# Optimization experiments

Hardware: AMD Instinct MI355X
Metric: run time of the kernel (lower is better)

## Reference

```python
import jax, jax.numpy as jnp
import numpy as np

FP8_MAX = 448.0      # max normal of float8_e4m3fn
BLOCK = 128          # TPUGEMMLinear.block_size default
INFO_THRESHOLD = 0.1
NUM_PATHS = 4


def act_quant(x, block=BLOCK):
    """Block-wise fp8 quantization along the last dim. Returns (q, scale) with
    q fp8_e4m3 of shape [..., n_blocks, block] and scale [..., n_blocks, 1]."""
    b = min(block, x.shape[-1])
    xb = x.reshape(*x.shape[:-1], x.shape[-1] // b, b)
    scale = jnp.max(jnp.abs(xb), axis=-1, keepdims=True) / FP8_MAX
    scale = jnp.maximum(scale, 1e-12)  # avoid div-by-zero
    xq = (xb / scale).astype(jnp.float8_e4m3fn)
    return xq, scale


def dequant(xq, scale, shape):
    return (xq.astype(jnp.float32) * scale).reshape(shape)


def quantize_roundtrip(x):
    xq, xs = act_quant(x)
    return dequant(xq, xs, x.shape)


def setup_inputs() -> dict:
    key = jax.random.key(0)
    k_x, k_ik, k_pk = jax.random.split(key, 3)
    N, D, F, P = 32768, 1024, 1024, NUM_PATHS
    Fp = F // P
    x = jax.random.normal(k_x, (N, D), dtype=jnp.float32)
    # lecun_normal init: std = 1/sqrt(fan_in)
    info_kernel = jax.random.normal(k_ik, (D, P), dtype=jnp.float32) / np.sqrt(D)
    info_bias = jnp.zeros((P,), dtype=jnp.float32)
    path_kernels = jax.random.normal(k_pk, (P, D, Fp), dtype=jnp.float32) / np.sqrt(D)
    path_biases = jnp.zeros((P, Fp), dtype=jnp.float32)
    return {"x": x, "info_kernel": info_kernel, "info_bias": info_bias,
            "path_kernels": path_kernels, "path_biases": path_biases}


def reference(x, info_kernel, info_bias, path_kernels, path_biases):
    N, D = x.shape
    P = info_kernel.shape[-1]
    # fp8 quantize/dequant round trips (simulated fp8 GEMM: dequant then matmul)
    xd = quantize_roundtrip(x)                      # [N, D]
    ikd = quantize_roundtrip(info_kernel)           # [D, P]
    pkd = quantize_roundtrip(path_kernels)          # [P, D, Fp]
    # info-gain gating
    info_net = xd @ ikd + info_bias                 # [N, P]
    info_gains = jax.nn.sigmoid(info_net)
    cumul_info = info_gains                         # prev_info defaults to zeros
    # training=True: soft path weights
    path_weights = jax.nn.sigmoid((cumul_info - INFO_THRESHOLD) * 10.0)  # [N, P]
    # per-path projections (batched GEMM) + per-path chunk weighting
    path_out = jnp.einsum('nd,pdf->npf', xd, pkd) + path_biases          # [N, P, Fp]
    out = (path_out * path_weights[:, :, None]).reshape(N, -1)           # [N, F]
    return out, cumul_info
```

## Files before the change

kernel.cpp:

```cpp
#include <hip/hip_runtime.h>
#include <hip/hip_bf16.h>
#include <stdint.h>


typedef float v2f __attribute__((ext_vector_type(2)));
typedef float f32x4 __attribute__((ext_vector_type(4)));
typedef __bf16 bf16x8 __attribute__((ext_vector_type(8)));
typedef unsigned short us4 __attribute__((ext_vector_type(4)));

__device__ __forceinline__ unsigned short f2bf(float f) {
  unsigned u = __builtin_bit_cast(unsigned, f);
  u += 0x7fffu + ((u >> 16) & 1u);
  return (unsigned short)(u >> 16);
}

__device__ __forceinline__ v2f fp8_rt2s(float a, float b, float sa, float sb) {
  int q = __builtin_amdgcn_cvt_pk_fp8_f32(a / sa, b / sb, 0, false);
  v2f r = __builtin_amdgcn_cvt_pk_f32_fp8(q, false);
  r.x *= sa;
  r.y *= sb;
  return r;
}

__device__ __forceinline__ void g2l16(const void* g, void* l) {
  __builtin_amdgcn_global_load_lds(
      (const __attribute__((address_space(1))) unsigned int*)g,
      (__attribute__((address_space(3))) unsigned int*)l,
      16, 0, 0);
}

__global__ __launch_bounds__(256) void k_quant_info(
    const float* __restrict__ x, const float* __restrict__ ik,
    const float* __restrict__ ib, unsigned short* __restrict__ xd,
    float* __restrict__ pw, float* __restrict__ cumul, int N) {
  __shared__ f32x4 s_ik[1024];
  const int tid = threadIdx.x;

  for (int d = tid; d < 1024; d += 256) {
    f32x4 v = ((const f32x4*)ik)[d];
    float m = fmaxf(fmaxf(fabsf(v.x), fabsf(v.y)), fmaxf(fabsf(v.z), fabsf(v.w)));
    float s = fmaxf(m * (1.0f / 448.0f), 1e-12f);
    v2f lo = fp8_rt2s(v.x, v.y, s, s);
    v2f hi = fp8_rt2s(v.z, v.w, s, s);
    f32x4 dq;
    dq.x = lo.x; dq.y = lo.y; dq.z = hi.x; dq.w = hi.y;
    s_ik[d] = dq;
  }
  __syncthreads();

  const int lane = tid & 63, wv = tid >> 6;
  const int gw = blockIdx.x * 4 + wv;
  const int nw = gridDim.x * 4;
  const f32x4 ibv = *(const f32x4*)ib;

  for (int row = gw; row < N; row += nw) {
    const f32x4* xr = (const f32x4*)(x + (size_t)row * 1024);
    float p0 = 0.f, p1 = 0.f, p2 = 0.f, p3 = 0.f;
#pragma unroll
    for (int j = 0; j < 4; ++j) {
      f32x4 v = xr[j * 64 + lane];
      float m = fmaxf(fmaxf(fabsf(v.x), fabsf(v.y)), fmaxf(fabsf(v.z), fabsf(v.w)));
#pragma unroll
      for (int off = 1; off <= 16; off <<= 1)
        m = fmaxf(m, __shfl_xor(m, off, 64));
      float s = fmaxf(m * (1.0f / 448.0f), 1e-12f);
      v2f lo = fp8_rt2s(v.x, v.y, s, s);
      v2f hi = fp8_rt2s(v.z, v.w, s, s);
      const int e = j * 256 + lane * 4;
      us4 h;
      h.x = f2bf(lo.x); h.y = f2bf(lo.y); h.z = f2bf(hi.x); h.w = f2bf(hi.y);
      *(us4*)(xd + (size_t)row * 1024 + e) = h;
      f32x4 k0 = s_ik[e], k1 = s_ik[e + 1], k2 = s_ik[e + 2], k3 = s_ik[e + 3];
      p0 += lo.x * k0.x + lo.y * k1.x + hi.x * k2.x + hi.y * k3.x;
      p1 += lo.x * k0.y + lo.y * k1.y + hi.x * k2.y + hi.y * k3.y;
      p2 += lo.x * k0.z + lo.y * k1.z + hi.x * k2.z + hi.y * k3.z;
      p3 += lo.x * k0.w + lo.y * k1.w + hi.x * k2.w + hi.y * k3.w;
    }
#pragma unroll
    for (int off = 1; off <= 32; off <<= 1) {
      p0 += __shfl_xor(p0, off, 64);
      p1 += __shfl_xor(p1, off, 64);
      p2 += __shfl_xor(p2, off, 64);
      p3 += __shfl_xor(p3, off, 64);
    }
    if (lane == 0) {
      float g0 = 1.f / (1.f + expf(-(p0 + ibv.x)));
      float g1 = 1.f / (1.f + expf(-(p1 + ibv.y)));
      float g2 = 1.f / (1.f + expf(-(p2 + ibv.z)));
      float g3 = 1.f / (1.f + expf(-(p3 + ibv.w)));
      f32x4 cg; cg.x = g0; cg.y = g1; cg.z = g2; cg.w = g3;
      *(f32x4*)(cumul + (size_t)row * 4) = cg;
      f32x4 w;
      w.x = 1.f / (1.f + expf(-((g0 - 0.1f) * 10.f)));
      w.y = 1.f / (1.f + expf(-((g1 - 0.1f) * 10.f)));
      w.z = 1.f / (1.f + expf(-((g2 - 0.1f) * 10.f)));
      w.w = 1.f / (1.f + expf(-((g3 - 0.1f) * 10.f)));
      *(f32x4*)(pw + (size_t)row * 4) = w;
    }
  }
}

__global__ __launch_bounds__(256) void k_quant_pk(
    const float* __restrict__ pk, unsigned short* __restrict__ bt) {
  __shared__ float s_x[32 * 256];
  __shared__ float s_s[32 * 2];
  const int tid = threadIdx.x;
  const int p = blockIdx.x >> 5;
  const int d0 = (blockIdx.x & 31) * 32;

  const f32x4* src = (const f32x4*)(pk + ((size_t)p * 1024 + d0) * 256);
  f32x4* dst = (f32x4*)s_x;
#pragma unroll
  for (int i = 0; i < 8; ++i) dst[tid + i * 256] = src[tid + i * 256];
  __syncthreads();

  {
    const int d = tid >> 3, seg = tid & 7;
    const float* rp = &s_x[d * 256 + seg * 32];
    float m = 0.f;
#pragma unroll
    for (int i = 0; i < 32; ++i) m = fmaxf(m, fabsf(rp[i]));
    m = fmaxf(m, __shfl_xor(m, 1, 64));
    m = fmaxf(m, __shfl_xor(m, 2, 64));
    if ((seg & 3) == 0) s_s[d * 2 + (seg >> 2)] = fmaxf(m * (1.0f / 448.0f), 1e-12f);
  }
  __syncthreads();

  const int f = tid;
  uint4 hv[4];
  unsigned* hw = (unsigned*)hv;
#pragma unroll
  for (int d = 0; d < 32; d += 2) {
    float v0 = s_x[d * 256 + f];
    float sa = s_s[d * 2 + (f >> 7)];
    float v1 = s_x[(d + 1) * 256 + f];
    float sb = s_s[(d + 1) * 2 + (f >> 7)];
    v2f r = fp8_rt2s(v0, v1, sa, sb);
    hw[d >> 1] = (unsigned)f2bf(r.x) | ((unsigned)f2bf(r.y) << 16);
  }
  unsigned short* orow = bt + (size_t)(p * 256 + f) * 1024 + d0;
  uint4* ov = (uint4*)orow;
#pragma unroll
  for (int i = 0; i < 4; ++i) ov[i] = hv[i];
}

__global__ __launch_bounds__(256) void k_gemm(
    const unsigned short* __restrict__ xd, const unsigned short* __restrict__ bt,
    const float* __restrict__ pb, const float* __restrict__ pw,
    float* __restrict__ out, int N) {
  __shared__ __align__(16) unsigned short As[128 * 64];
  __shared__ __align__(16) unsigned short Bs[128 * 64];
  const int tid = threadIdx.x;
  const int lane = tid & 63, wv = tid >> 6;
  const int bx = blockIdx.x;
  const int tm = bx >> 3, tn = bx & 7;
  const int m0 = tm * 128, f0 = tn * 128;
  const int wr = wv >> 1, wc = wv & 1;

  f32x4 acc[4][4] = {};
  const int frow = lane & 15;
  const int fk = (lane >> 4) * 8;

  for (int k0 = 0; k0 < 1024; k0 += 64) {
    __syncthreads();
#pragma unroll
    for (int i = 0; i < 4; ++i) {
      const int cbase = (wv * 4 + i) * 64;
      const int chunk = cbase + lane;
      const int r = chunk >> 3, c8 = chunk & 7;
      g2l16(xd + (size_t)(m0 + r) * 1024 + k0 + c8 * 8, (char*)As + cbase * 16);
      g2l16(bt + (size_t)(f0 + r) * 1024 + k0 + c8 * 8, (char*)Bs + cbase * 16);
    }
    __syncthreads();
#pragma unroll
    for (int kk = 0; kk < 64; kk += 32) {
      bf16x8 af[4], bfr[4];
#pragma unroll
      for (int mi = 0; mi < 4; ++mi)
        af[mi] = *(const bf16x8*)&As[(wr * 64 + mi * 16 + frow) * 64 + kk + fk];
#pragma unroll
      for (int ni = 0; ni < 4; ++ni)
        bfr[ni] = *(const bf16x8*)&Bs[(wc * 64 + ni * 16 + frow) * 64 + kk + fk];
#pragma unroll
      for (int mi = 0; mi < 4; ++mi)
#pragma unroll
        for (int ni = 0; ni < 4; ++ni)
          acc[mi][ni] = __builtin_amdgcn_mfma_f32_16x16x32_bf16(
              af[mi], bfr[ni], acc[mi][ni], 0, 0, 0);
    }
  }

  const int r0 = m0 + wr * 64 + (lane >> 4) * 4;
  const int c0 = f0 + wc * 64 + frow;
#pragma unroll
  for (int ni = 0; ni < 4; ++ni) {
    const int c = c0 + ni * 16;
    const float bias = pb[c];
    const int p = c >> 8;
#pragma unroll
    for (int mi = 0; mi < 4; ++mi) {
#pragma unroll
      for (int r = 0; r < 4; ++r) {
        const int row = r0 + mi * 16 + r;
        out[(size_t)row * 1024 + c] = (acc[mi][ni][r] + bias) * pw[row * 4 + p];
      }
    }
  }
}

extern "C" void kernel_launch(void* const* d_in, const int* in_sizes, int n_in,
                              void* d_out, int out_size, void* d_ws, size_t ws_size,
                              hipStream_t stream) {
  const float* x  = (const float*)d_in[0];
  const float* ik = (const float*)d_in[1];
  const float* ib = (const float*)d_in[2];
  const float* pk = (const float*)d_in[3];
  const float* pb = (const float*)d_in[4];
  const int N = in_sizes[0] / 1024;

  float* out = (float*)d_out;
  float* cumul = out + (size_t)N * 1024;

  char* ws = (char*)d_ws;
  unsigned short* xd = (unsigned short*)ws;
  unsigned short* bt = (unsigned short*)(ws + (size_t)N * 1024 * 2);
  float* pw = (float*)(ws + (size_t)N * 1024 * 2 + (size_t)1024 * 1024 * 2);

  hipLaunchKernelGGL(k_quant_info, dim3(2048), dim3(256), 0, stream,
                     x, ik, ib, xd, pw, cumul, N);
  hipLaunchKernelGGL(k_quant_pk, dim3(128), dim3(256), 0, stream, pk, bt);
  hipLaunchKernelGGL(k_gemm, dim3((N / 128) * 8), dim3(256), 0, stream,
                     xd, bt, pb, pw, out, N);
}
```

Before: 353.9 us.

## Keep info kernel in registers, fuse pk absmax into load, remap GEMM blocks per XCD

```diff
diff --git a/kernel.cpp b/kernel.cpp
--- a/kernel.cpp
+++ b/kernel.cpp
@@ -33,25 +33,28 @@
     const float* __restrict__ x, const float* __restrict__ ik,
     const float* __restrict__ ib, unsigned short* __restrict__ xd,
     float* __restrict__ pw, float* __restrict__ cumul, int N) {
-  __shared__ f32x4 s_ik[1024];
   const int tid = threadIdx.x;
-
-  for (int d = tid; d < 1024; d += 256) {
-    f32x4 v = ((const f32x4*)ik)[d];
-    float m = fmaxf(fmaxf(fabsf(v.x), fabsf(v.y)), fmaxf(fabsf(v.z), fabsf(v.w)));
-    float s = fmaxf(m * (1.0f / 448.0f), 1e-12f);
-    v2f lo = fp8_rt2s(v.x, v.y, s, s);
-    v2f hi = fp8_rt2s(v.z, v.w, s, s);
-    f32x4 dq;
-    dq.x = lo.x; dq.y = lo.y; dq.z = hi.x; dq.w = hi.y;
-    s_ik[d] = dq;
-  }
-  __syncthreads();
-
   const int lane = tid & 63, wv = tid >> 6;
   const int gw = blockIdx.x * 4 + wv;
   const int nw = gridDim.x * 4;
   const f32x4 ibv = *(const f32x4*)ib;
+
+  f32x4 kv[4][4];
+#pragma unroll
+  for (int j = 0; j < 4; ++j) {
+#pragma unroll
+    for (int q = 0; q < 4; ++q) {
+      const int d = j * 256 + lane * 4 + q;
+      f32x4 v = ((const f32x4*)ik)[d];
+      float m = fmaxf(fmaxf(fabsf(v.x), fabsf(v.y)), fmaxf(fabsf(v.z), fabsf(v.w)));
+      float s = fmaxf(m * (1.0f / 448.0f), 1e-12f);
+      v2f lo = fp8_rt2s(v.x, v.y, s, s);
+      v2f hi = fp8_rt2s(v.z, v.w, s, s);
+      f32x4 dq;
+      dq.x = lo.x; dq.y = lo.y; dq.z = hi.x; dq.w = hi.y;
+      kv[j][q] = dq;
+    }
+  }
 
   for (int row = gw; row < N; row += nw) {
     const f32x4* xr = (const f32x4*)(x + (size_t)row * 1024);
@@ -66,11 +69,10 @@
       float s = fmaxf(m * (1.0f / 448.0f), 1e-12f);
       v2f lo = fp8_rt2s(v.x, v.y, s, s);
       v2f hi = fp8_rt2s(v.z, v.w, s, s);
-      const int e = j * 256 + lane * 4;
       us4 h;
       h.x = f2bf(lo.x); h.y = f2bf(lo.y); h.z = f2bf(hi.x); h.w = f2bf(hi.y);
-      *(us4*)(xd + (size_t)row * 1024 + e) = h;
-      f32x4 k0 = s_ik[e], k1 = s_ik[e + 1], k2 = s_ik[e + 2], k3 = s_ik[e + 3];
+      *(us4*)(xd + (size_t)row * 1024 + j * 256 + lane * 4) = h;
+      f32x4 k0 = kv[j][0], k1 = kv[j][1], k2 = kv[j][2], k3 = kv[j][3];
       p0 += lo.x * k0.x + lo.y * k1.x + hi.x * k2.x + hi.y * k3.x;
       p1 += lo.x * k0.y + lo.y * k1.y + hi.x * k2.y + hi.y * k3.y;
       p2 += lo.x * k0.z + lo.y * k1.z + hi.x * k2.z + hi.y * k3.z;
@@ -105,24 +107,22 @@
   __shared__ float s_x[32 * 256];
   __shared__ float s_s[32 * 2];
   const int tid = threadIdx.x;
+  const int lane = tid & 63, wv = tid >> 6;
   const int p = blockIdx.x >> 5;
   const int d0 = (blockIdx.x & 31) * 32;
 
   const f32x4* src = (const f32x4*)(pk + ((size_t)p * 1024 + d0) * 256);
   f32x4* dst = (f32x4*)s_x;
 #pragma unroll
-  for (int i = 0; i < 8; ++i) dst[tid + i * 256] = src[tid + i * 256];
-  __syncthreads();
-
-  {
-    const int d = tid >> 3, seg = tid & 7;
-    const float* rp = &s_x[d * 256 + seg * 32];
-    float m = 0.f;
-#pragma unroll
-    for (int i = 0; i < 32; ++i) m = fmaxf(m, fabsf(rp[i]));
-    m = fmaxf(m, __shfl_xor(m, 1, 64));
-    m = fmaxf(m, __shfl_xor(m, 2, 64));
-    if ((seg & 3) == 0) s_s[d * 2 + (seg >> 2)] = fmaxf(m * (1.0f / 448.0f), 1e-12f);
+  for (int i = 0; i < 8; ++i) {
+    f32x4 v = src[tid + i * 256];
+    dst[tid + i * 256] = v;
+    float m = fmaxf(fmaxf(fabsf(v.x), fabsf(v.y)), fmaxf(fabsf(v.z), fabsf(v.w)));
+#pragma unroll
+    for (int off = 1; off <= 16; off <<= 1)
+      m = fmaxf(m, __shfl_xor(m, off, 64));
+    if ((lane & 31) == 0)
+      s_s[(wv + 4 * i) * 2 + (lane >> 5)] = fmaxf(m * (1.0f / 448.0f), 1e-12f);
   }
   __syncthreads();
 
@@ -152,7 +152,8 @@
   __shared__ __align__(16) unsigned short Bs[128 * 64];
   const int tid = threadIdx.x;
   const int lane = tid & 63, wv = tid >> 6;
-  const int bx = blockIdx.x;
+  const int nwg = gridDim.x, cpx = nwg >> 3;
+  const int bx = (blockIdx.x & 7) * cpx + (blockIdx.x >> 3);
   const int tm = bx >> 3, tn = bx & 7;
   const int m0 = tm * 128, f0 = tn * 128;
   const int wr = wv >> 1, wc = wv & 1;
```

Result: no change. 355.1 us (+0.4%).
